# Kernel tuning notes

Hardware: AMD Instinct MI355X
Metric: run time of the kernel (lower is better)

Reference implementation:

```python
import jax, jax.numpy as jnp
import numpy as np

HIDDEN = 256
GAMMA = 0.96875
SCALE_BASE = 512


def _rotate_every_two(x):
    x1 = x[..., ::2]
    x2 = x[..., 1::2]
    return jnp.stack((-x2, x1), axis=-1).reshape(x.shape)


def _xpos(x, downscale):
    # x: [B, H, L, D]; offset=0 path of XPOS._forward_impl
    L = x.shape[2]
    D = x.shape[-1]
    half = D // 2
    # buffer: (arange(0, D, 2) + 0.4*D) / (1.4*D)  -> [half]
    scale_vec = (jnp.arange(0, D, 2, dtype=jnp.float32) + 0.4 * D) / (1.4 * D)
    # scale ** (arange(L)/scale_base)[:, None] -> [L, half]
    exps = jnp.arange(L, dtype=jnp.float32) / SCALE_BASE
    scale = scale_vec[None, :] ** exps[:, None]
    # fixed_pos_embedding on scale (dim = half)
    inv_freq = 1.0 / (10000.0 ** (jnp.arange(half, dtype=jnp.float32) / half))
    sinusoid = jnp.arange(L, dtype=jnp.float32)[:, None] * inv_freq[None, :]  # [L, half]
    sin = jnp.sin(sinusoid)
    cos = jnp.cos(sinusoid)
    if downscale:
        scale = 1.0 / scale
    sin2 = jnp.repeat(sin * scale, 2, axis=-1)  # duplicate_interleave -> [L, D]
    cos2 = jnp.repeat(cos * scale, 2, axis=-1)
    return x * cos2 + _rotate_every_two(x) * sin2


def _decay_mask(L):
    n = jnp.arange(L)[:, None]
    m = jnp.arange(L)[None, :]
    return jnp.where(n >= m, jnp.power(GAMMA, (n - m).astype(jnp.float32)), 0.0)


def setup_inputs() -> dict:
    key = jax.random.key(0)
    k1, k2, k3, k4 = jax.random.split(key, 4)
    B, H, L, D = 8, 4, 2048, HIDDEN
    X = jax.random.normal(k1, (B, H, L, D), dtype=jnp.float32)
    W_Q = jax.random.normal(k2, (D, D), dtype=jnp.float32) / D
    W_K = jax.random.normal(k3, (D, D), dtype=jnp.float32) / D
    W_V = jax.random.normal(k4, (D, D), dtype=jnp.float32) / D
    return {"X": X, "W_Q": W_Q, "W_K": W_K, "W_V": W_V}


def reference(X, W_Q, W_K, W_V):
    L = X.shape[2]
    Q = X @ W_Q
    K = X @ W_K
    Q = _xpos(Q, downscale=False)
    K = _xpos(K, downscale=True)
    V = X @ W_V
    D = _decay_mask(L)  # [L, L]
    att = jnp.einsum('bhnd,bhmd->bhnm', Q, K) * D[None, None]
    return att @ V
```

## Files before the change

kernel.cpp:

```cpp
#include <hip/hip_runtime.h>
#include <stdint.h>

typedef unsigned short u16;
typedef unsigned int   u32;
typedef __attribute__((ext_vector_type(8))) short  bf16x8;
typedef __attribute__((ext_vector_type(4))) float  f32x4;
typedef __attribute__((ext_vector_type(4))) u32    u32x4;
typedef __attribute__((ext_vector_type(2))) u32    u32x2;

#define L_SEQ 2048
#define DMODEL 256

__device__ __forceinline__ u16 f2bf(float x){
  u32 u = __float_as_uint(x);
  return (u16)((u + 0x7FFFu + ((u >> 16) & 1u)) >> 16);
}

__device__ __forceinline__ u32 pack2(float a, float b){
  return (u32)f2bf(a) | ((u32)f2bf(b) << 16);
}

__device__ __forceinline__ void gload_lds16(const void* g, void* l){
  __builtin_amdgcn_global_load_lds(
      (const __attribute__((address_space(1))) u32*)g,
      (__attribute__((address_space(3))) u32*)l, 16, 0, 0);
}

__global__ void k_tables(float2* __restrict__ tq2, float2* __restrict__ tk2){
  int idx = blockIdx.x * 256 + threadIdx.x;
  int n = idx >> 7, hi = idx & 127;
  float fn = (float)n, fi = (float)hi;
  float invf = exp2f(-(fi * (1.0f/128.0f)) * 13.2877124f);
  float ang = fn * invf;
  float s = sinf(ang), c = cosf(ang);
  float sv = (2.0f * fi + 102.4f) * (1.0f / 358.4f);
  float sc = exp2f((fn * (1.0f/512.0f)) * log2f(sv));
  float2 q; q.x = c * sc;  q.y = s * sc;
  tq2[idx] = q;
  float inv = 1.0f / sc;
  float2 k; k.x = c * inv; k.y = s * inv;
  tk2[idx] = k;
}

__global__ void k_wt(const float* __restrict__ wq, const float* __restrict__ wk,
                     const float* __restrict__ wv, u16* __restrict__ wt2){
  int idx = blockIdx.x * 256 + threadIdx.x;
  int kc = idx / 6144, r = idx % 6144;
  int col = r >> 3, p = r & 7;
  int j = p ^ (col & 7);
  int wsel = col >> 8, c = col & 255;
  const float* src = (wsel == 0) ? wq : ((wsel == 1) ? wk : wv);
  int k0 = kc * 64 + j * 8;
  u32x4 v;
  v.x = pack2(src[(k0+0)*256 + c], src[(k0+1)*256 + c]);
  v.y = pack2(src[(k0+2)*256 + c], src[(k0+3)*256 + c]);
  v.z = pack2(src[(k0+4)*256 + c], src[(k0+5)*256 + c]);
  v.w = pack2(src[(k0+6)*256 + c], src[(k0+7)*256 + c]);
  *(u32x4*)(wt2 + (size_t)idx * 8) = v;
}

__global__ void k_xbf(const float* __restrict__ X, u16* __restrict__ Xb2){
  int idx = blockIdx.x * 256 + threadIdx.x;
  int row = idx >> 5, g = idx & 31;
  int kc = g >> 3, j = g & 7;
  int p = j ^ (row & 7);
  const float4* src = (const float4*)(X + (size_t)row * 256 + g * 8);
  float4 a = src[0], b = src[1];
  u32x4 v;
  v.x = pack2(a.x, a.y); v.y = pack2(a.z, a.w);
  v.z = pack2(b.x, b.y); v.w = pack2(b.z, b.w);
  *(u32x4*)(Xb2 + (((size_t)kc * 65536 + row) * 8 + p) * 8) = v;
}

__global__ __launch_bounds__(256, 2) void k_proj(
    const u16* __restrict__ Xb2, const u16* __restrict__ Wt2,
    const float2* __restrict__ tq2, const float2* __restrict__ tk2,
    u16* __restrict__ Qx, u16* __restrict__ Kx, u16* __restrict__ VT)
{
  __shared__ u16 ldsX[2][8192];
  __shared__ u16 ldsW[2][8192];
  const int p0 = blockIdx.x;
  const int l = (p0 & 7) * 384 + (p0 >> 3);
  const int ct = l % 6;
  const int rt = l / 6;
  const int wsel = ct >> 1;
  const int mcol0 = (ct & 1) * 128;
  const int row0 = rt * 128;
  const int bh = rt >> 4;
  const int tid = threadIdx.x;
  const int lane = tid & 63, wid = tid >> 6;
  const int h = lane >> 4, l15 = lane & 15;
  const int wrg = wid >> 1, wcg = wid & 1;

  f32x4 acc[4][4] = {};

  auto stage = [&](int kc, int buf){
    const u16* xsrc = Xb2 + ((size_t)kc * 65536 + row0) * 64;
    const u16* wsrc = Wt2 + ((size_t)kc * 768 + ct * 128) * 64;
#pragma unroll
    for (int t = 0; t < 4; ++t){
      int ci = t * 256 + tid;
      gload_lds16(xsrc + ci * 8, (char*)ldsX[buf] + (t * 256 + wid * 64) * 16);
      gload_lds16(wsrc + ci * 8, (char*)ldsW[buf] + (t * 256 + wid * 64) * 16);
    }
  };

  stage(0, 0);
  __syncthreads();

  for (int kc = 0; kc < 4; ++kc){
    const int cur = kc & 1;
    if (kc < 3) stage(kc + 1, cur ^ 1);

#pragma unroll
    for (int kb = 0; kb < 2; ++kb){
      bf16x8 xf[4], wf[4];
#pragma unroll
      for (int b = 0; b < 4; ++b){
        int r = wrg * 64 + b * 16 + l15;
        int p = (kb * 4 + h) ^ (r & 7);
        xf[b] = *(const bf16x8*)((const char*)ldsX[cur] + r * 128 + p * 16);
      }
#pragma unroll
      for (int a = 0; a < 4; ++a){
        int c = wcg * 64 + a * 16 + l15;
        int p = (kb * 4 + h) ^ (c & 7);
        wf[a] = *(const bf16x8*)((const char*)ldsW[cur] + c * 128 + p * 16);
      }
      if (wsel < 2){
#pragma unroll
        for (int a = 0; a < 4; ++a)
#pragma unroll
          for (int b = 0; b < 4; ++b)
            acc[a][b] = __builtin_amdgcn_mfma_f32_16x16x32_bf16(
                wf[a], xf[b], acc[a][b], 0, 0, 0);
      } else {
#pragma unroll
        for (int b = 0; b < 4; ++b)
#pragma unroll
          for (int a = 0; a < 4; ++a)
            acc[b][a] = __builtin_amdgcn_mfma_f32_16x16x32_bf16(
                xf[b], wf[a], acc[b][a], 0, 0, 0);
      }
    }
    __syncthreads();
  }

  if (wsel == 2){
#pragma unroll
    for (int b = 0; b < 4; ++b){
      int pos0 = (row0 + wrg * 64 + b * 16 + h * 4) & 2047;
#pragma unroll
      for (int a = 0; a < 4; ++a){
        int d = mcol0 + wcg * 64 + a * 16 + l15;
        f32x4 v = acc[b][a];
        u32x2 p2; p2.x = pack2(v.x, v.y); p2.y = pack2(v.z, v.w);
        *(u32x2*)(VT + ((size_t)bh * DMODEL + d) * 2048 + pos0) = p2;
      }
    }
  } else {
    const float2* tt = (wsel == 0) ? tq2 : tk2;
    u16* Od = (wsel == 0) ? Qx : Kx;
#pragma unroll
    for (int a = 0; a < 4; ++a){
      int d0 = mcol0 + wcg * 64 + a * 16 + h * 4;
#pragma unroll
      for (int b = 0; b < 4; ++b){
        int n = row0 + wrg * 64 + b * 16 + l15;
        int pos = n & 2047;
        f32x4 v = acc[a][b];
        float4 t = *(const float4*)(tt + pos * 128 + (d0 >> 1));
        float y0 = v.x * t.x - v.y * t.y;
        float y1 = v.y * t.x + v.x * t.y;
        float y2 = v.z * t.z - v.w * t.w;
        float y3 = v.w * t.z + v.z * t.w;
        u32x2 p2; p2.x = pack2(y0, y1); p2.y = pack2(y2, y3);
        *(u32x2*)(Od + (size_t)n * 256 + d0) = p2;
      }
    }
  }
}

__global__ __launch_bounds__(512) void k_attn(
    const u16* __restrict__ Qx, const u16* __restrict__ Kx,
    const u16* __restrict__ VT, float* __restrict__ out)
{
  __shared__ char smem[131072];

  const int pbid = blockIdx.x;
  const int bid = ((pbid & 7) << 6) | (pbid >> 3);
  const int bh = bid >> 4, i = bid & 15;
  const int tid = threadIdx.x;
  const int lane = tid & 63, w = tid >> 6;
  const int h = lane >> 4, l15 = lane & 15;
  const int n_g = i * 128 + w * 16 + l15;

  bf16x8 q[8];
  const u16* qbase = Qx + ((size_t)bh * 2048 + n_g) * 256;
#pragma unroll
  for (int kb = 0; kb < 8; ++kb)
    q[kb] = *(const bf16x8*)(qbase + kb * 32 + h * 8);

  f32x4 ot[16] = {};

  int j_lo = 2 * i - 4; if (j_lo < 0) j_lo = 0;
  const int j_hi = 2 * i + 1;
  const float L2G = -0.04580369f;
  const float GI1 = 1.03225806f;
  const float GI2 = 1.06555671f;
  const float GI3 = 1.09993040f;

  auto stage = [&](int j, int buf){
    const u16* kbase = Kx + ((size_t)bh * 2048 + j * 64) * 256;
    char* kdst = smem + buf * 32768;
#pragma unroll
    for (int t = 0; t < 4; ++t){
      int s = (w * 4 + t) * 64 + lane;
      int m = s >> 5, c = s & 31;
      gload_lds16(kbase + m * 256 + ((c ^ (m & 7)) * 8),
                  kdst + (w * 4 + t) * 1024);
    }
    const u16* vbase = VT + (size_t)bh * (DMODEL * 2048) + j * 64;
    char* vdst = smem + 65536 + buf * 32768;
#pragma unroll
    for (int t = 0; t < 4; ++t){
      int s = (w * 4 + t) * 64 + lane;
      int d = s >> 3, c = s & 7;
      gload_lds16(vbase + (size_t)d * 2048 + ((c ^ (d & 7)) * 8),
                  vdst + (w * 4 + t) * 1024);
    }
  };

  stage(j_lo, 0);
  __syncthreads();

  for (int j = j_lo; j <= j_hi; ++j){
    const int cur = (j - j_lo) & 1;
    if (j < j_hi) stage(j + 1, cur ^ 1);

    if (i * 128 + w * 16 + 15 >= j * 64){
      const char* ldsK = smem + cur * 32768;
      const char* ldsV = smem + 65536 + cur * 32768;
      f32x4 sacc[4] = {};
#pragma unroll
      for (int kb = 0; kb < 8; ++kb){
#pragma unroll
        for (int mt = 0; mt < 4; ++mt){
          int m = mt * 16 + l15;
          int chunk = kb * 4 + h;
          bf16x8 a = *(const bf16x8*)(ldsK + m * 512 +
                                      ((chunk ^ (m & 7)) * 16));
          sacc[mt] = __builtin_amdgcn_mfma_f32_16x16x32_bf16(
              a, q[kb], sacc[mt], 0, 0, 0);
        }
      }
      u32 dA[4], dB[4];
#pragma unroll
      for (int mt = 0; mt < 4; ++mt){
        int m0 = j * 64 + mt * 16 + h * 4;
        int dl = n_g - m0;
        float base = exp2f((float)dl * L2G);
        float v0 = (dl     >= 0) ? sacc[mt].x * base       : 0.0f;
        float v1 = (dl - 1 >= 0) ? sacc[mt].y * base * GI1 : 0.0f;
        float v2 = (dl - 2 >= 0) ? sacc[mt].z * base * GI2 : 0.0f;
        float v3 = (dl - 3 >= 0) ? sacc[mt].w * base * GI3 : 0.0f;
        dA[mt] = pack2(v0, v1);
        dB[mt] = pack2(v2, v3);
      }
      int s0 = l15 + 32 * (h & 1);
      int s1 = s0 + 16;
      bool lo = (h < 2);
#pragma unroll
      for (int kt = 0; kt < 2; ++kt){
        u32 a0 = (u32)__shfl((int)dA[2 * kt],     s0, 64);
        u32 a1 = (u32)__shfl((int)dA[2 * kt + 1], s0, 64);
        u32 b0 = (u32)__shfl((int)dB[2 * kt],     s0, 64);
        u32 b1 = (u32)__shfl((int)dB[2 * kt + 1], s0, 64);
        u32 a2 = (u32)__shfl((int)dA[2 * kt],     s1, 64);
        u32 a3 = (u32)__shfl((int)dA[2 * kt + 1], s1, 64);
        u32 b2 = (u32)__shfl((int)dB[2 * kt],     s1, 64);
        u32 b3 = (u32)__shfl((int)dB[2 * kt + 1], s1, 64);
        union { u32 u[4]; bf16x8 v; } uu;
        uu.u[0] = lo ? a0 : a1;
        uu.u[1] = lo ? b0 : b1;
        uu.u[2] = lo ? a2 : a3;
        uu.u[3] = lo ? b2 : b3;
        bf16x8 bfrag = uu.v;
#pragma unroll
        for (int dt = 0; dt < 16; ++dt){
          int d = dt * 16 + l15;
          int chunk = kt * 4 + h;
          bf16x8 a = *(const bf16x8*)(ldsV + d * 128 +
                                      ((chunk ^ (d & 7)) * 16));
          ot[dt] = __builtin_amdgcn_mfma_f32_16x16x32_bf16(
              a, bfrag, ot[dt], 0, 0, 0);
        }
      }
    }
    __syncthreads();
  }

  float* obase = out + ((size_t)bh * 2048 + n_g) * 256;
#pragma unroll
  for (int dt = 0; dt < 16; ++dt)
    *(f32x4*)(obase + dt * 16 + h * 4) = ot[dt];
}

extern "C" void kernel_launch(void* const* d_in, const int* in_sizes, int n_in,
                              void* d_out, int out_size, void* d_ws, size_t ws_size,
                              hipStream_t stream)
{
  (void)in_sizes; (void)n_in; (void)out_size; (void)ws_size;
  const float* X  = (const float*)d_in[0];
  const float* WQ = (const float*)d_in[1];
  const float* WK = (const float*)d_in[2];
  const float* WV = (const float*)d_in[3];
  float* out = (float*)d_out;

  char* ws = (char*)d_ws;
  float2* tq2 = (float2*)ws;
  float2* tk2 = (float2*)(ws + (2u << 20));
  u16* wt2 = (u16*)(ws + (4u << 20));
  u16* qx = (u16*)(ws + 4718592);
  u16* kx = (u16*)(ws + 38273024);
  u16* vt = (u16*)(ws + 71827456);

  u16* xb2 = (u16*)d_out;

  k_tables<<<dim3(1024), dim3(256), 0, stream>>>(tq2, tk2);
  k_wt<<<dim3(96), dim3(256), 0, stream>>>(WQ, WK, WV, wt2);
  k_xbf<<<dim3(8192), dim3(256), 0, stream>>>(X, xb2);
  k_proj<<<dim3(3072), dim3(256), 0, stream>>>(xb2, wt2, tq2, tk2, qx, kx, vt);
  k_attn<<<dim3(512), dim3(512), 0, stream>>>(qx, kx, vt, out);
}
```

Before: 139.7 us.

## Fuse X bf16 conversion into projection kernel and stage epilogue stores through LDS

Removes the separate X-to-bf16 conversion kernel. The projection kernel now loads fp32 X rows directly into registers, converts them, and writes them swizzled into LDS, with the next chunk's loads overlapped with the current MFMA work. The Q/K/V epilogues also stage results through LDS so global writes become coalesced 16-byte row stores, which matters most for the transposed V output. The cost is that each fp32 X tile is re-read by all six column tiles, doubling the X bytes per tile compared with bf16, and the epilogue gains extra register pressure and an extra barrier.

```diff
diff --git a/kernel.cpp b/kernel.cpp
--- a/kernel.cpp
+++ b/kernel.cpp
@@ -59,26 +59,12 @@
   *(u32x4*)(wt2 + (size_t)idx * 8) = v;
 }
 
-__global__ void k_xbf(const float* __restrict__ X, u16* __restrict__ Xb2){
-  int idx = blockIdx.x * 256 + threadIdx.x;
-  int row = idx >> 5, g = idx & 31;
-  int kc = g >> 3, j = g & 7;
-  int p = j ^ (row & 7);
-  const float4* src = (const float4*)(X + (size_t)row * 256 + g * 8);
-  float4 a = src[0], b = src[1];
-  u32x4 v;
-  v.x = pack2(a.x, a.y); v.y = pack2(a.z, a.w);
-  v.z = pack2(b.x, b.y); v.w = pack2(b.z, b.w);
-  *(u32x4*)(Xb2 + (((size_t)kc * 65536 + row) * 8 + p) * 8) = v;
-}
-
 __global__ __launch_bounds__(256, 2) void k_proj(
-    const u16* __restrict__ Xb2, const u16* __restrict__ Wt2,
+    const float* __restrict__ X, const u16* __restrict__ Wt2,
     const float2* __restrict__ tq2, const float2* __restrict__ tk2,
     u16* __restrict__ Qx, u16* __restrict__ Kx, u16* __restrict__ VT)
 {
-  __shared__ u16 ldsX[2][8192];
-  __shared__ u16 ldsW[2][8192];
+  __shared__ char smem[65536];
   const int p0 = blockIdx.x;
   const int l = (p0 & 7) * 384 + (p0 >> 3);
   const int ct = l % 6;
@@ -92,26 +78,50 @@
   const int h = lane >> 4, l15 = lane & 15;
   const int wrg = wid >> 1, wcg = wid & 1;
 
+  const int xr = tid >> 1;
+  const int xc4 = (tid & 1) * 4;
+
   f32x4 acc[4][4] = {};
 
-  auto stage = [&](int kc, int buf){
-    const u16* xsrc = Xb2 + ((size_t)kc * 65536 + row0) * 64;
+  float4 xl[8];
+  auto loadX = [&](int kc){
+    const float4* src = (const float4*)(X + (size_t)(row0 + xr) * 256 +
+                                        kc * 64 + xc4 * 8);
+#pragma unroll
+    for (int j = 0; j < 8; ++j) xl[j] = src[j];
+  };
+  auto writeX = [&](int buf){
+    char* dst = smem + buf * 16384 + xr * 128;
+#pragma unroll
+    for (int j = 0; j < 4; ++j){
+      float4 a = xl[2*j], b = xl[2*j+1];
+      u32x4 v;
+      v.x = pack2(a.x, a.y); v.y = pack2(a.z, a.w);
+      v.z = pack2(b.x, b.y); v.w = pack2(b.z, b.w);
+      *(u32x4*)(dst + (((xc4 + j) ^ (xr & 7)) * 16)) = v;
+    }
+  };
+  auto stageW = [&](int kc, int buf){
     const u16* wsrc = Wt2 + ((size_t)kc * 768 + ct * 128) * 64;
+    char* dst = smem + 32768 + buf * 16384;
 #pragma unroll
     for (int t = 0; t < 4; ++t){
       int ci = t * 256 + tid;
-      gload_lds16(xsrc + ci * 8, (char*)ldsX[buf] + (t * 256 + wid * 64) * 16);
-      gload_lds16(wsrc + ci * 8, (char*)ldsW[buf] + (t * 256 + wid * 64) * 16);
+      gload_lds16(wsrc + ci * 8, dst + (t * 256 + wid * 64) * 16);
     }
   };
 
-  stage(0, 0);
+  loadX(0);
+  stageW(0, 0);
+  writeX(0);
   __syncthreads();
 
   for (int kc = 0; kc < 4; ++kc){
     const int cur = kc & 1;
-    if (kc < 3) stage(kc + 1, cur ^ 1);
-
+    if (kc < 3){ loadX(kc + 1); stageW(kc + 1, cur ^ 1); }
+
+    const char* lX = smem + cur * 16384;
+    const char* lW = smem + 32768 + cur * 16384;
 #pragma unroll
     for (int kb = 0; kb < 2; ++kb){
       bf16x8 xf[4], wf[4];
@@ -119,13 +129,13 @@
       for (int b = 0; b < 4; ++b){
         int r = wrg * 64 + b * 16 + l15;
         int p = (kb * 4 + h) ^ (r & 7);
-        xf[b] = *(const bf16x8*)((const char*)ldsX[cur] + r * 128 + p * 16);
+        xf[b] = *(const bf16x8*)(lX + r * 128 + p * 16);
       }
 #pragma unroll
       for (int a = 0; a < 4; ++a){
         int c = wcg * 64 + a * 16 + l15;
         int p = (kb * 4 + h) ^ (c & 7);
-        wf[a] = *(const bf16x8*)((const char*)ldsW[cur] + c * 128 + p * 16);
+        wf[a] = *(const bf16x8*)(lW + c * 128 + p * 16);
       }
       if (wsel < 2){
 #pragma unroll
@@ -143,22 +153,11 @@
                 xf[b], wf[a], acc[b][a], 0, 0, 0);
       }
     }
+    if (kc < 3) writeX(cur ^ 1);
     __syncthreads();
   }
 
-  if (wsel == 2){
-#pragma unroll
-    for (int b = 0; b < 4; ++b){
-      int pos0 = (row0 + wrg * 64 + b * 16 + h * 4) & 2047;
-#pragma unroll
-      for (int a = 0; a < 4; ++a){
-        int d = mcol0 + wcg * 64 + a * 16 + l15;
-        f32x4 v = acc[b][a];
-        u32x2 p2; p2.x = pack2(v.x, v.y); p2.y = pack2(v.z, v.w);
-        *(u32x2*)(VT + ((size_t)bh * DMODEL + d) * 2048 + pos0) = p2;
-      }
-    }
-  } else {
+  if (wsel < 2){
     const float2* tt = (wsel == 0) ? tq2 : tk2;
     u16* Od = (wsel == 0) ? Qx : Kx;
 #pragma unroll
@@ -175,7 +174,49 @@
         float y2 = v.z * t.z - v.w * t.w;
         float y3 = v.w * t.z + v.z * t.w;
         u32x2 p2; p2.x = pack2(y0, y1); p2.y = pack2(y2, y3);
-        *(u32x2*)(Od + (size_t)n * 256 + d0) = p2;
+        int lrow = wrg * 64 + b * 16 + l15;
+        int lcolb = (wcg * 64 + a * 16 + h * 4) * 2;
+        *(u32x2*)(smem + lrow * 256 + (lcolb ^ ((lrow & 7) << 4))) = p2;
+      }
+    }
+    __syncthreads();
+    {
+      const int r = tid >> 1;
+      const int cbase = (tid & 1) * 8;
+      u16* orow = Od + (size_t)(row0 + r) * 256 + mcol0 + cbase * 8;
+#pragma unroll
+      for (int j = 0; j < 8; ++j){
+        int c16 = cbase + j;
+        u32x4 v = *(const u32x4*)(smem + r * 256 +
+                                  ((c16 * 16) ^ ((r & 7) << 4)));
+        *(u32x4*)(orow + j * 8) = v;
+      }
+    }
+  } else {
+#pragma unroll
+    for (int b = 0; b < 4; ++b){
+      int lpos = wrg * 64 + b * 16 + h * 4;
+#pragma unroll
+      for (int a = 0; a < 4; ++a){
+        int ld = wcg * 64 + a * 16 + l15;
+        f32x4 v = acc[b][a];
+        u32x2 p2; p2.x = pack2(v.x, v.y); p2.y = pack2(v.z, v.w);
+        *(u32x2*)(smem + ld * 256 + ((lpos * 2) ^ ((ld & 7) << 4))) = p2;
+      }
+    }
+    __syncthreads();
+    {
+      const int dloc = tid >> 1;
+      const int cbase = (tid & 1) * 8;
+      const int posbase = (rt & 15) * 128;
+      u16* orow = VT + ((size_t)bh * DMODEL + mcol0 + dloc) * 2048 +
+                  posbase + cbase * 8;
+#pragma unroll
+      for (int j = 0; j < 8; ++j){
+        int c16 = cbase + j;
+        u32x4 v = *(const u32x4*)(smem + dloc * 256 +
+                                  ((c16 * 16) ^ ((dloc & 7) << 4)));
+        *(u32x4*)(orow + j * 8) = v;
       }
     }
   }
@@ -325,11 +366,8 @@
   u16* kx = (u16*)(ws + 38273024);
   u16* vt = (u16*)(ws + 71827456);
 
-  u16* xb2 = (u16*)d_out;
-
   k_tables<<<dim3(1024), dim3(256), 0, stream>>>(tq2, tk2);
   k_wt<<<dim3(96), dim3(256), 0, stream>>>(WQ, WK, WV, wt2);
-  k_xbf<<<dim3(8192), dim3(256), 0, stream>>>(X, xb2);
-  k_proj<<<dim3(3072), dim3(256), 0, stream>>>(xb2, wt2, tq2, tk2, qx, kx, vt);
+  k_proj<<<dim3(3072), dim3(256), 0, stream>>>(X, wt2, tq2, tk2, qx, kx, vt);
   k_attn<<<dim3(512), dim3(512), 0, stream>>>(qx, kx, vt, out);
 }
```

Measured after the change: 159.4 us. 1.14x slower.
